# Kernel tuning notes

Hardware: AMD Instinct MI355X
Metric: run time of the kernel (lower is better)

## Reference

```python
import jax, jax.numpy as jnp
import numpy as np
import math

D_MODEL = 1024
N_HEADS = 16
D_HEAD = 64
D_MLP = 4096
INIT_RANGE = 0.02
VAR_EPS = 1e-05
BATCH = 2
SEQ = 2048


def new_gelu(x):
    c = math.sqrt(2.0 / math.pi)
    return 0.5 * x * (1.0 + jnp.tanh(c * (x + 0.044715 * x ** 3)))


def layer_norm(x, w, b):
    mean = jnp.mean(x, axis=-1, keepdims=True)
    x = x - mean
    var = jnp.mean(x * x, axis=-1, keepdims=True)
    return x / jnp.sqrt(var + VAR_EPS) * w + b


def setup_inputs() -> dict:
    key = jax.random.key(0)
    ks = jax.random.split(key, 12)
    s = INIT_RANGE
    return {
        "resid": jax.random.normal(ks[0], (BATCH, SEQ, D_MODEL), jnp.float32),
        "w_q": s * jax.random.normal(ks[1], (N_HEADS, D_MODEL, D_HEAD), jnp.float32),
        "w_k": s * jax.random.normal(ks[2], (N_HEADS, D_MODEL, D_HEAD), jnp.float32),
        "w_v": s * jax.random.normal(ks[3], (N_HEADS, D_MODEL, D_HEAD), jnp.float32),
        "w_o": s * jax.random.normal(ks[4], (N_HEADS, D_HEAD, D_MODEL), jnp.float32),
        "ln1_w": s * jax.random.normal(ks[5], (D_MODEL,), jnp.float32),
        "ln1_b": jnp.zeros((D_MODEL,), jnp.float32),
        "ln2_w": s * jax.random.normal(ks[6], (D_MODEL,), jnp.float32),
        "ln2_b": jnp.zeros((D_MODEL,), jnp.float32),
        "w_in": s * jax.random.normal(ks[7], (D_MODEL, D_MLP), jnp.float32),
        "b_in": jnp.zeros((D_MLP,), jnp.float32),
        "w_out": s * jax.random.normal(ks[8], (D_MLP, D_MODEL), jnp.float32),
        "b_out": jnp.zeros((D_MODEL,), jnp.float32),
    }


def attention(x, w_q, w_k, w_v, w_o):
    # x: [b, s, d]; weights: [h, d, dh] / [h, dh, d]
    qs = jnp.einsum('bsd,hde->bhse', x, w_q)
    ks = jnp.einsum('bsd,hde->bhse', x, w_k)
    vs = jnp.einsum('bsd,hde->bhse', x, w_v)
    attn = jnp.einsum('bhqe,bhke->bhqk', qs, ks)  # [b, h, s, s]
    s = attn.shape[-1]
    causal = jnp.triu(jnp.ones((s, s), dtype=bool), k=1)
    attn = jnp.where(causal, -jnp.inf, attn)
    attn = jax.nn.softmax(attn / math.sqrt(D_HEAD), axis=-1)
    z = jnp.einsum('bhqk,bhke->bhqe', attn, vs)
    return jnp.einsum('bhse,hed->bsd', z, w_o)


def reference(resid, w_q, w_k, w_v, w_o, ln1_w, ln1_b, ln2_w, ln2_b, w_in, b_in, w_out, b_out):
    resid = resid + attention(layer_norm(resid, ln1_w, ln1_b), w_q, w_k, w_v, w_o)
    h = layer_norm(resid, ln2_w, ln2_b)
    h = new_gelu(jnp.einsum('bsd,dm->bsm', h, w_in) + b_in)
    resid = resid + jnp.einsum('bsm,md->bsd', h, w_out) + b_out
    return resid
```

## Files before the change

kernel.cpp:

```cpp
#include <hip/hip_runtime.h>

#define DEV static __device__ __forceinline__

typedef unsigned short u16;
typedef __attribute__((ext_vector_type(8))) __bf16 bf16x8;
typedef __attribute__((ext_vector_type(4))) float f32x4;

DEV float bf2f(u16 u) { union { unsigned int i; float f; } v; v.i = ((unsigned int)u) << 16; return v.f; }
DEV u16 f2bf(float f) {
  union { float f; unsigned int i; } v; v.f = f;
  unsigned int r = v.i + 0x7fffu + ((v.i >> 16) & 1u);
  return (u16)(r >> 16);
}

DEV float gelu_f(float x) {
  float u = 0.7978845608028654f * (x + 0.044715f * x * x * x);
  float e = __expf(2.f * u);
  float t = 1.f - 2.f / (e + 1.f);
  return 0.5f * x * (1.f + t);
}

DEV void async16(const u16* g, u16* l) {
  __builtin_amdgcn_global_load_lds(
      (const __attribute__((address_space(1))) unsigned int*)g,
      (__attribute__((address_space(3))) unsigned int*)l, 16, 0, 0);
}

__global__ __launch_bounds__(256) void transpose_all(
    const float* __restrict__ w_q, const float* __restrict__ w_k,
    const float* __restrict__ w_v, const float* __restrict__ w_o,
    const float* __restrict__ w_in, const float* __restrict__ w_out,
    u16* __restrict__ WQKVT, u16* __restrict__ WOT,
    u16* __restrict__ WINT, u16* __restrict__ WOUTT)
{
  int t = blockIdx.x;
  const float* src; u16* dst; int R, C, c0, r0;
  if (t < 3072) {
    int seg = t >> 10, tt = t & 1023;
    int z = tt >> 6, rem = tt & 63;
    const float* w = seg == 0 ? w_q : (seg == 1 ? w_k : w_v);
    src = w + z * 65536;
    dst = WQKVT + seg * 1048576 + z * 65536;
    R = 1024; C = 64;
    c0 = (rem >> 5) * 32; r0 = (rem & 31) * 32;
  } else if (t < 4096) {
    int tt = t - 3072;
    src = w_o; dst = WOT; R = 1024; C = 1024;
    c0 = (tt & 31) * 32; r0 = (tt >> 5) * 32;
  } else if (t < 8192) {
    int tt = t - 4096;
    src = w_in; dst = WINT; R = 1024; C = 4096;
    c0 = (tt & 127) * 32; r0 = (tt >> 7) * 32;
  } else {
    int tt = t - 8192;
    src = w_out; dst = WOUTT; R = 4096; C = 1024;
    c0 = (tt & 31) * 32; r0 = (tt >> 5) * 32;
  }
  __shared__ float tile[32][33];
  int tx = threadIdx.x & 31, ty = threadIdx.x >> 5;
#pragma unroll
  for (int i = 0; i < 32; i += 8)
    tile[ty + i][tx] = src[(size_t)(r0 + ty + i) * C + (c0 + tx)];
  __syncthreads();
#pragma unroll
  for (int i = 0; i < 32; i += 8)
    dst[(size_t)(c0 + ty + i) * R + (r0 + tx)] = f2bf(tile[tx][ty + i]);
}

__global__ __launch_bounds__(256) void ln_kernel(
    const float* __restrict__ x, const float* __restrict__ g,
    const float* __restrict__ b, u16* __restrict__ out)
{
  int row = blockIdx.x, tid = threadIdx.x;
  const float4 v = ((const float4*)(x + (size_t)row * 1024))[tid];
  float s = v.x + v.y + v.z + v.w;
  float ss = v.x * v.x + v.y * v.y + v.z * v.z + v.w * v.w;
#pragma unroll
  for (int m = 1; m < 64; m <<= 1) { s += __shfl_xor(s, m, 64); ss += __shfl_xor(ss, m, 64); }
  __shared__ float red[8];
  if ((tid & 63) == 0) { red[tid >> 6] = s; red[4 + (tid >> 6)] = ss; }
  __syncthreads();
  s = red[0] + red[1] + red[2] + red[3];
  ss = red[4] + red[5] + red[6] + red[7];
  float mean = s * (1.f / 1024.f);
  float var = ss * (1.f / 1024.f) - mean * mean;
  float rstd = rsqrtf(var + 1e-5f);
  float4 gv = ((const float4*)g)[tid];
  float4 bv = ((const float4*)b)[tid];
  u16* o = out + (size_t)row * 1024 + tid * 4;
  o[0] = f2bf((v.x - mean) * rstd * gv.x + bv.x);
  o[1] = f2bf((v.y - mean) * rstd * gv.y + bv.y);
  o[2] = f2bf((v.z - mean) * rstd * gv.z + bv.z);
  o[3] = f2bf((v.w - mean) * rstd * gv.w + bv.w);
}

template <int EPI, int BM, int BN>
__global__ __launch_bounds__(256) void gemm_bf16(
    const u16* __restrict__ A, const u16* __restrict__ Bt, int K, int N,
    const float* __restrict__ addv, const float* __restrict__ bias,
    float* __restrict__ outF, u16* __restrict__ o0, u16* __restrict__ o1,
    u16* __restrict__ o2)
{
  constexpr int IM = BM / 32, IN = BN / 32;
  __shared__ u16 lA[2][BM * 64];
  __shared__ u16 lB[2][BN * 64];
  const int tid = threadIdx.x;
  const int lane = tid & 63, wave = tid >> 6;
  const int wm = wave >> 1, wn = wave & 1;
  const int quad = lane >> 4, l16 = lane & 15;
  const int m0 = blockIdx.y * BM, n0 = blockIdx.x * BN;

  f32x4 acc[IM][IN] = {};

  const int srow = lane >> 3;
  const int soff = ((lane & 7) ^ srow) << 3;

  auto stage = [&](int bsel, int kt) {
#pragma unroll
    for (int q = 0; q < BM / 32; ++q) {
      int rbase = wave * (BM / 4) + q * 8;
      async16(A + (size_t)(m0 + rbase + srow) * K + kt + soff, lA[bsel] + rbase * 64);
    }
#pragma unroll
    for (int q = 0; q < BN / 32; ++q) {
      int rbase = wave * (BN / 4) + q * 8;
      async16(Bt + (size_t)(n0 + rbase + srow) * K + kt + soff, lB[bsel] + rbase * 64);
    }
  };

  stage(0, 0);
  int buf = 0;

  for (int kt = 0; kt < K; kt += 64) {
    __syncthreads();
    if (kt + 64 < K) stage(buf ^ 1, kt + 64);
    const u16* cA = lA[buf];
    const u16* cB = lB[buf];
#pragma unroll
    for (int kk = 0; kk < 2; ++kk) {
      bf16x8 af[IM], bfr[IN];
#pragma unroll
      for (int i = 0; i < IM; ++i) {
        int ar = wm * (BM / 2) + i * 16 + l16;
        af[i] = *(const bf16x8*)&cA[ar * 64 + ((((kk * 4) + quad) ^ (ar & 7)) << 3)];
      }
#pragma unroll
      for (int j = 0; j < IN; ++j) {
        int br = wn * (BN / 2) + j * 16 + l16;
        bfr[j] = *(const bf16x8*)&cB[br * 64 + ((((kk * 4) + quad) ^ (br & 7)) << 3)];
      }
#pragma unroll
      for (int i = 0; i < IM; ++i)
#pragma unroll
        for (int j = 0; j < IN; ++j)
          acc[i][j] = __builtin_amdgcn_mfma_f32_16x16x32_bf16(af[i], bfr[j], acc[i][j], 0, 0, 0);
    }
    buf ^= 1;
  }

#pragma unroll
  for (int i = 0; i < IM; ++i) {
    const int rowb = m0 + wm * (BM / 2) + i * 16 + quad * 4;
#pragma unroll
    for (int j = 0; j < IN; ++j) {
      const int col = n0 + wn * (BN / 2) + j * 16 + l16;
#pragma unroll
      for (int rr = 0; rr < 4; ++rr) {
        const int m = rowb + rr;
        const float v = acc[i][j][rr];
        if (EPI == 0) {
          int bb = m >> 11, s = m & 2047;
          int proj = col >> 10, hc = col & 1023, hh = hc >> 6, e = hc & 63;
          size_t bhh = (size_t)(bb * 16 + hh);
          if (proj == 0) o0[(bhh * 2048 + s) * 64 + e] = f2bf(v * 0.125f);
          else if (proj == 1) o1[(bhh * 2048 + s) * 64 + e] = f2bf(v);
          else o2[bhh * 131072 + (size_t)e * 2048 + s] = f2bf(v);
        } else if (EPI == 1) {
          size_t idx = (size_t)m * N + col;
          outF[idx] = v + addv[idx];
        } else if (EPI == 2) {
          o0[(size_t)m * N + col] = f2bf(gelu_f(v + bias[col]));
        } else {
          size_t idx = (size_t)m * N + col;
          outF[idx] = v + bias[col] + addv[idx];
        }
      }
    }
  }
}

__global__ __launch_bounds__(256) void attn_flash(
    const u16* __restrict__ Q, const u16* __restrict__ K,
    const u16* __restrict__ Vt, u16* __restrict__ Z)
{
  __shared__ u16 lK[2][64 * 64];
  __shared__ u16 lV[2][64 * 64];
  __shared__ u16 lP[4][16 * 64];

  const int tid = threadIdx.x;
  const int lane = tid & 63, wave = tid >> 6;
  const int quad = lane >> 4, l16 = lane & 15;

  const int flat = blockIdx.x;
  const int xcd = flat & 7, w = flat >> 3;
  const int bhid = xcd * 4 + (w >> 4);
  const int p = w & 15;
  const int b = bhid >> 4, h = bhid & 15;
  const size_t bh = (size_t)bhid;

  const int nA = 32 - p;
  const int q0A = (31 - p) * 64;
  const int q0B = p * 64;

  const int srow = lane >> 3;
  const int soff = ((lane & 7) ^ srow) << 3;

  u16* myP = lP[wave];

  auto stage = [&](int buf, int s) {
    int kt0 = (s < nA ? s : s - nA) * 64;
#pragma unroll
    for (int q = 0; q < 2; ++q) {
      int rbase = wave * 16 + q * 8;
      async16(K + (bh * 2048 + (size_t)(kt0 + rbase + srow)) * 64 + soff,
              lK[buf] + rbase * 64);
      async16(Vt + bh * 131072 + (size_t)(rbase + srow) * 2048 + kt0 + soff,
              lV[buf] + rbase * 64);
    }
  };

  stage(0, 0);

  f32x4 oacc[4] = {};
  float lrow[4] = {};
  int q0w = q0A + wave * 16;

  bf16x8 qf[2];
#pragma unroll
  for (int d = 0; d < 2; ++d)
    qf[d] = *(const bf16x8*)(Q + (bh * 2048 + (size_t)(q0w + l16)) * 64 + d * 32 + quad * 8);

  auto writeO = [&]() {
#pragma unroll
    for (int rr = 0; rr < 4; ++rr) {
      float l = lrow[rr];
#pragma unroll
      for (int msk = 1; msk < 16; msk <<= 1) l += __shfl_xor(l, msk, 64);
      lrow[rr] = 1.f / l;
    }
#pragma unroll
    for (int d = 0; d < 4; ++d)
#pragma unroll
      for (int rr = 0; rr < 4; ++rr) {
        int srowq = q0w + quad * 4 + rr;
        Z[((size_t)(b * 2048 + srowq)) * 1024 + h * 64 + d * 16 + l16] =
            f2bf(oacc[d][rr] * lrow[rr]);
      }
  };

  for (int s = 0; s < 33; ++s) {
    if (s == nA) {
      writeO();
#pragma unroll
      for (int d = 0; d < 4; ++d)
#pragma unroll
        for (int e = 0; e < 4; ++e) oacc[d][e] = 0.f;
#pragma unroll
      for (int rr = 0; rr < 4; ++rr) lrow[rr] = 0.f;
      q0w = q0B + wave * 16;
#pragma unroll
      for (int d = 0; d < 2; ++d)
        qf[d] = *(const bf16x8*)(Q + (bh * 2048 + (size_t)(q0w + l16)) * 64 + d * 32 + quad * 8);
    }

    __syncthreads();
    if (s < 32) stage((s + 1) & 1, s + 1);

    const u16* cK = lK[s & 1];
    const u16* cV = lV[s & 1];
    const int kt0 = (s < nA ? s : s - nA) * 64;

    bf16x8 kf[4][2];
#pragma unroll
    for (int j = 0; j < 4; ++j)
#pragma unroll
      for (int d = 0; d < 2; ++d) {
        int key = j * 16 + l16;
        kf[j][d] = *(const bf16x8*)(cK + key * 64 + (((d * 4 + quad) ^ (key & 7)) << 3));
      }
    f32x4 sv[4];
#pragma unroll
    for (int j = 0; j < 4; ++j) {
      f32x4 z = {};
      z = __builtin_amdgcn_mfma_f32_16x16x32_bf16(qf[0], kf[j][0], z, 0, 0, 0);
      z = __builtin_amdgcn_mfma_f32_16x16x32_bf16(qf[1], kf[j][1], z, 0, 0, 0);
      sv[j] = z;
    }

    const bool needMask = (kt0 + 63 > q0w);
#pragma unroll
    for (int rr = 0; rr < 4; ++rr) {
      int rowl = quad * 4 + rr;
      int rowg = q0w + rowl;
      u16* prow = myP + rowl * 64;
      float accl = lrow[rr];
#pragma unroll
      for (int j = 0; j < 4; ++j) {
        float pv = __expf(sv[j][rr]);
        if (needMask && (kt0 + j * 16 + l16 > rowg)) pv = 0.f;
        accl += pv;
        int chk = j * 2 + (l16 >> 3);
        prow[((chk ^ (rowl & 7)) << 3) + (l16 & 7)] = (u16)(__float_as_uint(pv) >> 16);
      }
      lrow[rr] = accl;
    }

#pragma unroll
    for (int ks = 0; ks < 2; ++ks) {
      int chk = ks * 4 + quad;
      bf16x8 pf, vf[4];
      pf = *(const bf16x8*)(myP + l16 * 64 + ((chk ^ (l16 & 7)) << 3));
#pragma unroll
      for (int d = 0; d < 4; ++d) {
        int dh = d * 16 + l16;
        vf[d] = *(const bf16x8*)(cV + dh * 64 + ((chk ^ (dh & 7)) << 3));
      }
#pragma unroll
      for (int d = 0; d < 4; ++d)
        oacc[d] = __builtin_amdgcn_mfma_f32_16x16x32_bf16(pf, vf[d], oacc[d], 0, 0, 0);
    }
  }

  writeO();
}

extern "C" void kernel_launch(void* const* d_in, const int* in_sizes, int n_in,
                              void* d_out, int out_size, void* d_ws, size_t ws_size,
                              hipStream_t stream) {
  const float* resid = (const float*)d_in[0];
  const float* w_q  = (const float*)d_in[1];
  const float* w_k  = (const float*)d_in[2];
  const float* w_v  = (const float*)d_in[3];
  const float* w_o  = (const float*)d_in[4];
  const float* ln1w = (const float*)d_in[5];
  const float* ln1b = (const float*)d_in[6];
  const float* ln2w = (const float*)d_in[7];
  const float* ln2b = (const float*)d_in[8];
  const float* w_in = (const float*)d_in[9];
  const float* b_in = (const float*)d_in[10];
  const float* w_out= (const float*)d_in[11];
  const float* b_out= (const float*)d_in[12];
  float* out = (float*)d_out;

  const size_t MB = 1u << 20;
  char* ws = (char*)d_ws;
  u16* WQKVT = (u16*)(ws + 0);
  u16* WOT   = (u16*)(ws + 6 * MB);
  u16* WINT  = (u16*)(ws + 8 * MB);
  u16* WOUTT = (u16*)(ws + 16 * MB);
  u16* X1    = (u16*)(ws + 24 * MB);
  u16* Qb    = (u16*)(ws + 32 * MB);
  u16* Kb    = (u16*)(ws + 40 * MB);
  u16* Vb    = (u16*)(ws + 48 * MB);
  u16* Zb    = (u16*)(ws + 56 * MB);
  float* R2  = (float*)(ws + 64 * MB);
  u16* Hb    = (u16*)(ws + 80 * MB);
  u16* Gb    = (u16*)(ws + 24 * MB);

  transpose_all<<<dim3(12288), 256, 0, stream>>>(w_q, w_k, w_v, w_o, w_in, w_out,
                                                 WQKVT, WOT, WINT, WOUTT);
  ln_kernel<<<4096, 256, 0, stream>>>(resid, ln1w, ln1b, X1);
  gemm_bf16<0, 128, 64><<<dim3(48, 32), 256, 0, stream>>>(X1, WQKVT, 1024, 3072, nullptr, nullptr, nullptr, Qb, Kb, Vb);
  attn_flash<<<dim3(512), 256, 0, stream>>>(Qb, Kb, Vb, Zb);
  gemm_bf16<1, 128, 64><<<dim3(16, 32), 256, 0, stream>>>(Zb, WOT, 1024, 1024, resid, nullptr, R2, nullptr, nullptr, nullptr);
  ln_kernel<<<4096, 256, 0, stream>>>(R2, ln2w, ln2b, Hb);
  gemm_bf16<2, 128, 64><<<dim3(64, 32), 256, 0, stream>>>(Hb, WINT, 1024, 4096, nullptr, b_in, nullptr, Gb, nullptr, nullptr);
  gemm_bf16<3, 128, 64><<<dim3(16, 32), 256, 0, stream>>>(Gb, WOUTT, 4096, 1024, R2, b_out, out, nullptr, nullptr, nullptr);
}
```

Baseline: 352.8 us.

## Deepen GEMM prefetch to two stages in flight and remap blocks for locality

Restructures the bf16 GEMM main loop so two k-tiles are issued up front. Each iteration waits with a partial vmcnt so the next tile's global-to-LDS loads stay in flight while MFMAs run, and the freed buffer is refilled after a second barrier. It also permutes the flat block index across groups of eight, meant to improve L2 or cache reuse of A/B tiles. The hand-coded vmcnt literal is tied to BM=128/BN=64, enforced by static_assert, which breaks any other tile instantiation. Note that stage(1,64) is issued even when K is 64.

```diff
diff --git a/kernel.cpp b/kernel.cpp
--- a/kernel.cpp
+++ b/kernel.cpp
@@ -101,6 +101,7 @@
     float* __restrict__ outF, u16* __restrict__ o0, u16* __restrict__ o1,
     u16* __restrict__ o2)
 {
+  static_assert(BM == 128 && BN == 64, "vmcnt literal assumes 6 loads/wave/stage");
   constexpr int IM = BM / 32, IN = BN / 32;
   __shared__ u16 lA[2][BM * 64];
   __shared__ u16 lB[2][BN * 64];
@@ -108,7 +109,13 @@
   const int lane = tid & 63, wave = tid >> 6;
   const int wm = wave >> 1, wn = wave & 1;
   const int quad = lane >> 4, l16 = lane & 15;
-  const int m0 = blockIdx.y * BM, n0 = blockIdx.x * BN;
+
+  const int nwg = gridDim.x * gridDim.y;
+  int flat = blockIdx.x + gridDim.x * blockIdx.y;
+  flat = (flat & 7) * (nwg >> 3) + (flat >> 3);
+  const int bx = flat % gridDim.x;
+  const int by = flat / gridDim.x;
+  const int m0 = by * BM, n0 = bx * BN;
 
   f32x4 acc[IM][IN] = {};
 
@@ -128,14 +135,19 @@
     }
   };
 
+  const int T = K >> 6;
   stage(0, 0);
-  int buf = 0;
-
-  for (int kt = 0; kt < K; kt += 64) {
-    __syncthreads();
-    if (kt + 64 < K) stage(buf ^ 1, kt + 64);
-    const u16* cA = lA[buf];
-    const u16* cB = lB[buf];
+  stage(1, 64);
+
+  for (int t = 0; t < T; ++t) {
+    if (t == T - 1)
+      asm volatile("s_waitcnt vmcnt(0)" ::: "memory");
+    else
+      asm volatile("s_waitcnt vmcnt(6)" ::: "memory");
+    __builtin_amdgcn_s_barrier();
+
+    const u16* cA = lA[t & 1];
+    const u16* cB = lB[t & 1];
 #pragma unroll
     for (int kk = 0; kk < 2; ++kk) {
       bf16x8 af[IM], bfr[IN];
@@ -155,7 +167,12 @@
         for (int j = 0; j < IN; ++j)
           acc[i][j] = __builtin_amdgcn_mfma_f32_16x16x32_bf16(af[i], bfr[j], acc[i][j], 0, 0, 0);
     }
-    buf ^= 1;
+
+    if (t + 2 < T) {
+      asm volatile("s_waitcnt lgkmcnt(0)" ::: "memory");
+      __builtin_amdgcn_s_barrier();
+      stage(t & 1, (t + 2) << 6);
+    }
   }
 
 #pragma unroll
```

Measured after the change: 360.5 us. 2.2% more time.
